# Performance work log

Measured on AMD Instinct MI355X. Metric: run time of the kernel, lower is better.

## Reference

```python
import jax, jax.numpy as jnp
import numpy as np

M_MARGIN = 0.25
GAMMA = 256.0
NEG_INF = jnp.float32(-1e30)


def setup_inputs() -> dict:
    key = jax.random.key(0)
    k1, k2 = jax.random.split(key)
    feature = jax.random.normal(k1, (8192, 128), dtype=jnp.float32)
    label = jax.random.randint(k2, (8192,), 0, 64, dtype=jnp.int64)
    return {"feature": feature, "label": label}


def reference(feature, label):
    # F.normalize: L2-normalize rows (eps=1e-12)
    norm = jnp.maximum(jnp.linalg.norm(feature, axis=1, keepdims=True), 1e-12)
    f = feature / norm
    sim = f @ f.T  # [N, N]
    N = sim.shape[0]

    same = label[:, None] == label[None, :]
    triu = jnp.triu(jnp.ones((N, N), dtype=bool), k=1)
    pos_mask = same & triu
    neg_mask = (~same) & triu

    sim_d = jax.lax.stop_gradient(sim)  # .detach() in original
    ap = jnp.maximum(-sim_d + 1.0 + M_MARGIN, 0.0)
    an = jnp.maximum(sim_d + M_MARGIN, 0.0)
    delta_p = 1.0 - M_MARGIN
    delta_n = M_MARGIN

    logit_p = -ap * (sim - delta_p) * GAMMA
    logit_n = an * (sim - delta_n) * GAMMA

    # boolean-gather + logsumexp == masked logsumexp (fixed shapes, jit-friendly)
    lse_p = jax.nn.logsumexp(jnp.where(pos_mask, logit_p, NEG_INF))
    lse_n = jax.nn.logsumexp(jnp.where(neg_mask, logit_n, NEG_INF))

    return jax.nn.softplus(lse_n + lse_p)
```

## Files before the change

### kernel.cpp

```cpp
#include <hip/hip_runtime.h>
#include <hip/hip_bf16.h>
#include <math.h>

#define NROW 8192
#define DIM  128
#define BM   128
#define BN   128
#define NT   (NROW / BM)
#define NTILES ((NT * (NT + 1)) / 2)

typedef __bf16 bf16x8 __attribute__((ext_vector_type(8)));
typedef float  f32x4  __attribute__((ext_vector_type(4)));

#define G2      369.3299304675746f
#define NEGBIG  (-3.0e38f)
#define NOFF    2000.0f

__global__ __launch_bounds__(256)
void prep_kernel(const float* __restrict__ f, __hip_bfloat16* __restrict__ fhi) {
    int row  = blockIdx.x * 4 + (threadIdx.x >> 6);
    int lane = threadIdx.x & 63;
    float2 v = ((const float2*)(f + (size_t)row * DIM))[lane];
    float ss = v.x * v.x + v.y * v.y;
    #pragma unroll
    for (int off = 32; off; off >>= 1) ss += __shfl_xor(ss, off, 64);
    float inv = 1.0f / fmaxf(sqrtf(ss), 1e-12f);
    __hip_bfloat162 hv;
    hv.x = __float2bfloat16(v.x * inv);
    hv.y = __float2bfloat16(v.y * inv);
    ((__hip_bfloat162*)(fhi + (size_t)row * DIM))[lane] = hv;
}

__global__ __launch_bounds__(256, 4)
void sim_kernel(const __hip_bfloat16* __restrict__ fhi,
                const int* __restrict__ lab,
                float4* __restrict__ blockRes) {
    const int tid  = threadIdx.x;
    const int w    = tid >> 6;
    const int lane = tid & 63;
    const int lrow = lane & 15;
    const int lk   = lane >> 4;

    int bid = blockIdx.x;
    int tr = (int)((129.0f - sqrtf(16641.0f - 8.0f * (float)bid)) * 0.5f);
    while (tr > 0 && bid < tr * NT - (tr * (tr - 1)) / 2) --tr;
    while (bid >= (tr + 1) * NT - ((tr + 1) * tr) / 2) ++tr;
    const int tc = tr + (bid - (tr * NT - (tr * (tr - 1)) / 2));

    const int rowBase = tr * BM;
    const int colBase = tc * BN;

    __shared__ __align__(16) char smem[2 * 16384];
    __shared__ int labA[BM];
    __shared__ int labB[BN];
    __shared__ float red[4][4];

    if (tid < BM) labA[tid] = lab[rowBase + tid];
    else          labB[tid - BM] = lab[colBase + (tid - BM)];

    f32x4 acc[4][4];
    #pragma unroll
    for (int mi = 0; mi < 4; ++mi)
        #pragma unroll
        for (int ni = 0; ni < 4; ++ni) acc[mi][ni] = (f32x4){0.f, 0.f, 0.f, 0.f};

    const int mrow0 = (w >> 1) * 64;
    const int ncol0 = (w & 1) * 64;

    const int rsub = lane >> 3;
    const int kbs  = 16 * ((lane & 7) ^ rsub);

    for (int kc = 0; kc < 2; ++kc) {
        #pragma unroll
        for (int t = 0; t < 8; ++t) {
            int seg = w * 8 + t;
            int arr = seg >> 4;
            int s16 = seg & 15;
            char* ldsb = smem + arr * 16384 + s16 * 1024;
            int grow = (arr ? colBase : rowBase) + s16 * 8 + rsub;
            const char* g = (const char*)fhi + (size_t)grow * 256 + kc * 128 + kbs;
            __builtin_amdgcn_global_load_lds(
                (const __attribute__((address_space(1))) void*)g,
                (__attribute__((address_space(3))) void*)ldsb, 16, 0, 0);
        }
        __syncthreads();

        const char* As = smem;
        const char* Bs = smem + 16384;
        #pragma unroll
        for (int c = 0; c < 2; ++c) {
            int kb = c * 64 + lk * 16;
            bf16x8 bfr[4];
            #pragma unroll
            for (int ni = 0; ni < 4; ++ni) {
                int rb = ncol0 + ni * 16 + lrow;
                bfr[ni] = *(const bf16x8*)(Bs + rb * 128 + (kb ^ ((rb & 7) << 4)));
            }
            #pragma unroll
            for (int mi = 0; mi < 4; ++mi) {
                int ra = mrow0 + mi * 16 + lrow;
                bf16x8 afr = *(const bf16x8*)(As + ra * 128 + (kb ^ ((ra & 7) << 4)));
                #pragma unroll
                for (int ni = 0; ni < 4; ++ni)
                    acc[mi][ni] = __builtin_amdgcn_mfma_f32_16x16x32_bf16(afr, bfr[ni], acc[mi][ni], 0, 0, 0);
            }
        }
        __syncthreads();
    }

    float mp = NEGBIG, mn2 = NEGBIG;
    const bool diag = (tr == tc);

    int lbv[4];
    #pragma unroll
    for (int ni = 0; ni < 4; ++ni) lbv[ni] = labB[ncol0 + ni * 16 + lrow];

    #pragma unroll
    for (int mi = 0; mi < 4; ++mi) {
        const int il0 = mrow0 + mi * 16 + lk * 4;
        int4 la4 = *(const int4*)&labA[il0];
        const int la[4] = {la4.x, la4.y, la4.z, la4.w};
        #pragma unroll
        for (int ni = 0; ni < 4; ++ni) {
            const int jl = ncol0 + ni * 16 + lrow;
            #pragma unroll
            for (int r = 0; r < 4; ++r) {
                float s = acc[mi][ni][r];
                bool pos = (la[r] == lbv[ni]);
                float lp = fmaxf(1.25f - s, 0.f) * fmaf(-G2, s, 0.75f * G2);
                float ln2v = fmaf(fmaxf(s + 0.25f, 0.f), fmaf(G2, s, -0.25f * G2), -NOFF);
                if (diag) {
                    bool valid = (jl > il0 + r);
                    lp   = valid ? lp   : NEGBIG;
                    ln2v = valid ? ln2v : NEGBIG;
                }
                mp  = fmaxf(mp,  pos ? lp : NEGBIG);
                mn2 = fmaxf(mn2, pos ? NEGBIG : ln2v);
                acc[mi][ni][r] = pos ? lp : ln2v;
            }
        }
    }

    #pragma unroll
    for (int off = 32; off; off >>= 1) {
        mp  = fmaxf(mp,  __shfl_xor(mp,  off, 64));
        mn2 = fmaxf(mn2, __shfl_xor(mn2, off, 64));
    }
    if (lane == 0) { red[w][0] = mp; red[w][1] = mn2; }
    __syncthreads();
    const float Mp  = fmaxf(fmaxf(red[0][0], red[1][0]), fmaxf(red[2][0], red[3][0]));
    const float Mn2 = fmaxf(fmaxf(red[0][1], red[1][1]), fmaxf(red[2][1], red[3][1]));

    float sp = 0.f, sn = 0.f;
    #pragma unroll
    for (int mi = 0; mi < 4; ++mi)
        #pragma unroll
        for (int ni = 0; ni < 4; ++ni)
            #pragma unroll
            for (int r = 0; r < 4; ++r) {
                float x = acc[mi][ni][r];
                bool pos = (x > -1000.f);
                float m = pos ? Mp : Mn2;
                float e = __builtin_amdgcn_exp2f(x - m);
                float ep = pos ? e : 0.f;
                sp += ep;
                sn += (e - ep);
            }

    #pragma unroll
    for (int off = 32; off; off >>= 1) {
        sp += __shfl_xor(sp, off, 64);
        sn += __shfl_xor(sn, off, 64);
    }
    if (lane == 0) { red[w][2] = sp; red[w][3] = sn; }
    __syncthreads();
    if (tid == 0) {
        float Sp = red[0][2] + red[1][2] + red[2][2] + red[3][2];
        float Sn = red[0][3] + red[1][3] + red[2][3] + red[3][3];
        blockRes[bid] = make_float4(Mp, Sp, Mn2, Sn);
    }
}

__device__ __forceinline__ void merge2(float& m, float& s, float mo, float so) {
    float M = fmaxf(m, mo);
    s = s * __builtin_amdgcn_exp2f(m - M) + so * __builtin_amdgcn_exp2f(mo - M);
    m = M;
}

__global__ __launch_bounds__(256)
void finalize_kernel(const float4* __restrict__ blockRes, float* __restrict__ out) {
    __shared__ float red[4][4];
    int tid = threadIdx.x;
    float mp = NEGBIG, sp = 0.f, mn = NEGBIG, sn = 0.f;
    for (int i = tid; i < NTILES; i += 256) {
        float4 v = blockRes[i];
        merge2(mp, sp, v.x, v.y);
        merge2(mn, sn, v.z, v.w);
    }
    #pragma unroll
    for (int off = 32; off; off >>= 1) {
        float mo = __shfl_xor(mp, off, 64), so = __shfl_xor(sp, off, 64);
        merge2(mp, sp, mo, so);
        float mo2 = __shfl_xor(mn, off, 64), so2 = __shfl_xor(sn, off, 64);
        merge2(mn, sn, mo2, so2);
    }
    int wv = tid >> 6;
    if ((tid & 63) == 0) {
        red[wv][0] = mp; red[wv][1] = sp; red[wv][2] = mn; red[wv][3] = sn;
    }
    __syncthreads();
    if (tid == 0) {
        mp = red[0][0]; sp = red[0][1]; mn = red[0][2]; sn = red[0][3];
        #pragma unroll
        for (int q = 1; q < 4; ++q) {
            merge2(mp, sp, red[q][0], red[q][1]);
            merge2(mn, sn, red[q][2], red[q][3]);
        }
        const double LN2 = 0.6931471805599453;
        double lse_p = ((double)mp + log2((double)sp)) * LN2;
        double lse_n = ((double)mn + (double)NOFF + log2((double)sn)) * LN2;
        double xx = lse_p + lse_n;
        double r = (xx > 30.0) ? xx : log1p(exp(xx));
        out[0] = (float)r;
    }
}

extern "C" void kernel_launch(void* const* d_in, const int* in_sizes, int n_in,
                              void* d_out, int out_size, void* d_ws, size_t ws_size,
                              hipStream_t stream) {
    const float* f   = (const float*)d_in[0];
    const int*   lab = (const int*)d_in[1];
    float*  out      = (float*)d_out;

    __hip_bfloat16* fhi = (__hip_bfloat16*)d_ws;
    float4* blockRes    = (float4*)((char*)d_ws + 4u * 1024 * 1024);

    prep_kernel<<<NROW / 4, 256, 0, stream>>>(f, fhi);
    sim_kernel<<<NTILES, 256, 0, stream>>>(fhi, lab, blockRes);
    finalize_kernel<<<1, 256, 0, stream>>>(blockRes, out);
}
```

Before: 49.82 us.

## Load full K into LDS upfront and simplify logit computation algebraically

Issues all global-to-LDS loads for both K chunks before a single barrier, which doubles shared memory to 64KB and removes the per-chunk synchronisation. The epilogue folds the piecewise positive/negative logit formulas into one quadratic with selected coefficients, uses a single combined max, and computes two exp2 per element instead of one. The larger LDS footprint may lower occupancy, and the extra exp per element adds VALU work.

```diff
diff --git a/kernel.cpp b/kernel.cpp
--- a/kernel.cpp
+++ b/kernel.cpp
@@ -50,7 +50,7 @@
     const int rowBase = tr * BM;
     const int colBase = tc * BN;
 
-    __shared__ __align__(16) char smem[2 * 16384];
+    __shared__ __align__(16) char smem[4 * 16384];
     __shared__ int labA[BM];
     __shared__ int labB[BN];
     __shared__ float red[4][4];
@@ -70,23 +70,25 @@
     const int rsub = lane >> 3;
     const int kbs  = 16 * ((lane & 7) ^ rsub);
 
+    #pragma unroll
+    for (int t = 0; t < 16; ++t) {
+        int sg  = w * 16 + t;
+        int arr = sg >> 4;
+        int s16 = sg & 15;
+        int kc  = arr >> 1;
+        char* ldsb = smem + arr * 16384 + s16 * 1024;
+        int grow = ((arr & 1) ? colBase : rowBase) + s16 * 8 + rsub;
+        const char* g = (const char*)fhi + (size_t)grow * 256 + kc * 128 + kbs;
+        __builtin_amdgcn_global_load_lds(
+            (const __attribute__((address_space(1))) void*)g,
+            (__attribute__((address_space(3))) void*)ldsb, 16, 0, 0);
+    }
+    __syncthreads();
+
+    #pragma unroll
     for (int kc = 0; kc < 2; ++kc) {
-        #pragma unroll
-        for (int t = 0; t < 8; ++t) {
-            int seg = w * 8 + t;
-            int arr = seg >> 4;
-            int s16 = seg & 15;
-            char* ldsb = smem + arr * 16384 + s16 * 1024;
-            int grow = (arr ? colBase : rowBase) + s16 * 8 + rsub;
-            const char* g = (const char*)fhi + (size_t)grow * 256 + kc * 128 + kbs;
-            __builtin_amdgcn_global_load_lds(
-                (const __attribute__((address_space(1))) void*)g,
-                (__attribute__((address_space(3))) void*)ldsb, 16, 0, 0);
-        }
-        __syncthreads();
-
-        const char* As = smem;
-        const char* Bs = smem + 16384;
+        const char* As = smem + kc * 32768;
+        const char* Bs = As + 16384;
         #pragma unroll
         for (int c = 0; c < 2; ++c) {
             int kb = c * 64 + lk * 16;
@@ -105,10 +107,12 @@
                     acc[mi][ni] = __builtin_amdgcn_mfma_f32_16x16x32_bf16(afr, bfr[ni], acc[mi][ni], 0, 0, 0);
             }
         }
-        __syncthreads();
-    }
-
-    float mp = NEGBIG, mn2 = NEGBIG;
+    }
+
+    const float Ppos = -2.0f * G2;
+    const float Qpos = 0.9375f * G2;
+    const float Qneg = -0.0625f * G2 - NOFF;
+    float mall = NEGBIG, mneg = NEGBIG;
     const bool diag = (tr == tc);
 
     int lbv[4];
@@ -127,29 +131,31 @@
             for (int r = 0; r < 4; ++r) {
                 float s = acc[mi][ni][r];
                 bool pos = (la[r] == lbv[ni]);
-                float lp = fmaxf(1.25f - s, 0.f) * fmaf(-G2, s, 0.75f * G2);
-                float ln2v = fmaf(fmaxf(s + 0.25f, 0.f), fmaf(G2, s, -0.25f * G2), -NOFF);
-                if (diag) {
-                    bool valid = (jl > il0 + r);
-                    lp   = valid ? lp   : NEGBIG;
-                    ln2v = valid ? ln2v : NEGBIG;
-                }
-                mp  = fmaxf(mp,  pos ? lp : NEGBIG);
-                mn2 = fmaxf(mn2, pos ? NEGBIG : ln2v);
-                acc[mi][ni][r] = pos ? lp : ln2v;
+                float P  = pos ? Ppos : 0.0f;
+                float Qc = pos ? Qpos : Qneg;
+                float base = fmaf(G2, s * s, fmaf(P, s, Qc));
+                bool keep = pos || (s > -0.25f);
+                float x = keep ? base : -NOFF;
+                if (diag) x = (jl > il0 + r) ? x : NEGBIG;
+                mall = fmaxf(mall, x);
+                float xn = pos ? NEGBIG : x;
+                mneg = fmaxf(mneg, xn);
+                acc[mi][ni][r] = x;
             }
         }
     }
 
     #pragma unroll
     for (int off = 32; off; off >>= 1) {
-        mp  = fmaxf(mp,  __shfl_xor(mp,  off, 64));
-        mn2 = fmaxf(mn2, __shfl_xor(mn2, off, 64));
-    }
-    if (lane == 0) { red[w][0] = mp; red[w][1] = mn2; }
-    __syncthreads();
-    const float Mp  = fmaxf(fmaxf(red[0][0], red[1][0]), fmaxf(red[2][0], red[3][0]));
-    const float Mn2 = fmaxf(fmaxf(red[0][1], red[1][1]), fmaxf(red[2][1], red[3][1]));
+        mall = fmaxf(mall, __shfl_xor(mall, off, 64));
+        mneg = fmaxf(mneg, __shfl_xor(mneg, off, 64));
+    }
+    if (lane == 0) { red[w][0] = mall; red[w][1] = mneg; }
+    __syncthreads();
+    const float mar = fmaxf(fmaxf(red[0][0], red[1][0]), fmaxf(red[2][0], red[3][0]));
+    const float mnr = fmaxf(fmaxf(red[0][1], red[1][1]), fmaxf(red[2][1], red[3][1]));
+    const float Mp  = (mar > -1000.f) ? mar : 0.f;
+    const float Mn2 = (mnr > -2500.f) ? mnr : -1000.f;
 
     float sp = 0.f, sn = 0.f;
     #pragma unroll
@@ -159,12 +165,9 @@
             #pragma unroll
             for (int r = 0; r < 4; ++r) {
                 float x = acc[mi][ni][r];
-                bool pos = (x > -1000.f);
-                float m = pos ? Mp : Mn2;
-                float e = __builtin_amdgcn_exp2f(x - m);
-                float ep = pos ? e : 0.f;
-                sp += ep;
-                sn += (e - ep);
+                sp += __builtin_amdgcn_exp2f(x - Mp);
+                float xm = (x > -1000.f) ? NEGBIG : x;
+                sn += __builtin_amdgcn_exp2f(xm - Mn2);
             }
 
     #pragma unroll
@@ -172,6 +175,7 @@
         sp += __shfl_xor(sp, off, 64);
         sn += __shfl_xor(sn, off, 64);
     }
+    __syncthreads();
     if (lane == 0) { red[w][2] = sp; red[w][3] = sn; }
     __syncthreads();
     if (tid == 0) {
```

Measured after the change: 48.67 us. 2.3% less time.
